# Performance work log

Hardware: AMD Instinct MI355X
Metric: run time of the kernel (lower is better)

Reference implementation:

```python
import jax, jax.numpy as jnp
import numpy as np

B, N_IN, K_OUT, C_IN, C_OUT = 32, 2048, 128, 16, 16
NUM_ITERS = 3


def squash_v1(x, axis):
    s2 = (x ** 2).sum(axis, keepdims=True)
    return (jnp.sqrt(s2) / (0.5 + s2)) * x


def setup_inputs() -> dict:
    key = jax.random.key(0)
    k1, k2, k3 = jax.random.split(key, 3)
    x = jax.random.normal(k1, (B, N_IN, C_IN), dtype=jnp.float32)
    y = jax.random.normal(k2, (B, K_OUT), dtype=jnp.float32)  # unused by forward
    labels = jnp.arange(K_OUT, dtype=jnp.int64)
    # xavier-uniform-ish init for W1 [N_in, K_out, out_ch, in_ch] (leading 1 dropped)
    bound = float(np.sqrt(6.0 / (C_IN + C_OUT)))
    W1 = jax.random.uniform(k3, (N_IN, K_OUT, C_OUT, C_IN), dtype=jnp.float32,
                            minval=-bound, maxval=bound)
    return {"x": x, "y": y, "labels": labels, "W1": W1}


def reference(x, y, labels, W1):
    # select output capsules, then u_hat[b,i,k,d] = sum_c W[i,k,d,c] * x[b,i,c]
    W = W1[:, labels]                                   # [N, K, D, C]
    u_hat = jnp.einsum('ikdc,bic->bikd', W, x)          # [B, N, K, D]
    u_sq = squash_v1(u_hat, axis=-1)                    # reused each iteration
    b = jnp.zeros(u_hat.shape[:3], dtype=u_hat.dtype)   # [B, N, K]
    v = None
    for i in range(NUM_ITERS):
        c = jax.nn.softmax(b, axis=2)                   # over output capsules
        c = c / c.sum(axis=1, keepdims=True)            # normalize over input caps
        v = squash_v1(jnp.einsum('bik,bikd->bkd', c, u_hat), axis=-1)  # [B, K, D]
        if i < NUM_ITERS - 1:
            dd = 1.0 - ((u_sq - v[:, None]) ** 2).sum(-1)  # [B, N, K]
            b = b + dd
    poses = v                                           # [B, K, D]
    activations = jnp.sqrt((poses ** 2).sum(-1))        # [B, K]
    return poses, activations
```

## Files before the change

### kernel.cpp

```cpp
#include <hip/hip_runtime.h>


typedef __attribute__((ext_vector_type(8))) short  s16x8;
typedef __attribute__((ext_vector_type(4))) float  f32x4;

__device__ __forceinline__ unsigned bf16rn(float f) {
    const unsigned u = __builtin_bit_cast(unsigned, f);
    return (u + 0x7fffu + ((u >> 16) & 1u)) >> 16;
}
__device__ __forceinline__ unsigned pack2rn(float a, float b) {
    return bf16rn(a) | (bf16rn(b) << 16);
}
__device__ __forceinline__ unsigned phi(float a, float b) {
    return (__builtin_bit_cast(unsigned, a) >> 16) | (__builtin_bit_cast(unsigned, b) & 0xffff0000u);
}
__device__ __forceinline__ unsigned plo(float a, float b) {
    const float la = a - __builtin_bit_cast(float, __builtin_bit_cast(unsigned, a) & 0xffff0000u);
    const float lb = b - __builtin_bit_cast(float, __builtin_bit_cast(unsigned, b) & 0xffff0000u);
    return pack2rn(la, lb);
}

__device__ __forceinline__ void pack_A(const float* __restrict__ xp, s16x8& A1, s16x8& A2) {
    const float4 x0 = *(const float4*)xp;
    const float4 x1 = *(const float4*)(xp + 4);
    uint4 h, l;
    h.x = phi(x0.x, x0.y); h.y = phi(x0.z, x0.w);
    h.z = phi(x1.x, x1.y); h.w = phi(x1.z, x1.w);
    l.x = plo(x0.x, x0.y); l.y = plo(x0.z, x0.w);
    l.z = plo(x1.x, x1.y); l.w = plo(x1.z, x1.w);
    A1 = __builtin_bit_cast(s16x8, h);
    A2 = __builtin_bit_cast(s16x8, l);
}

__device__ __forceinline__ s16x8 pack_B_f(const float4 w0, const float4 w1, bool sel) {
    const float f[8] = {w0.x, w0.y, w0.z, w0.w, w1.x, w1.y, w1.z, w1.w};
    float t[8];
#pragma unroll
    for (int j = 0; j < 8; ++j) {
        const float hf = __builtin_bit_cast(float, __builtin_bit_cast(unsigned, f[j]) & 0xffff0000u);
        t[j] = sel ? hf : (f[j] - hf);
    }
    uint4 bw;
    bw.x = pack2rn(t[0], t[1]);
    bw.y = pack2rn(t[2], t[3]);
    bw.z = pack2rn(t[4], t[5]);
    bw.w = pack2rn(t[6], t[7]);
    return __builtin_bit_cast(s16x8, bw);
}
__device__ __forceinline__ s16x8 pack_B(const float* __restrict__ wp, bool sel) {
    return pack_B_f(*(const float4*)wp, *(const float4*)(wp + 4), sel);
}

__global__ __launch_bounds__(256) void k_packX(const float* __restrict__ x,
                                               s16x8* __restrict__ xA)
{
    const int wid  = blockIdx.x * 4 + (threadIdx.x >> 6);
    const int lane = threadIdx.x & 63;
    const int i  = wid >> 1, bg = wid & 1;
    const int n  = lane & 15, q = lane >> 4;
    const int oct = (q & 1) * 8;
    s16x8 A1, A2;
    pack_A(x + ((size_t)(bg * 16 + n) * 2048 + i) * 16 + oct, A1, A2);
    s16x8* o = xA + ((size_t)wid * 64 + lane) * 2;
    o[0] = A1;
    o[1] = A2;
}

__global__ __launch_bounds__(256) void k_packWacc(const float* __restrict__ W,
                                                  const s16x8* __restrict__ xA,
                                                  s16x8* __restrict__ Wp,
                                                  float* __restrict__ out_sl)
{
    const int w    = blockIdx.x * 4 + (threadIdx.x >> 6);
    const int lane = threadIdx.x & 63;
    const int n    = lane & 15;
    const int q    = lane >> 4;
    const int oct  = (q & 1) * 8;
    const bool sel = (q < 2);
    const int k0    = (w & 63) * 2;
    const int slice = w >> 6;
    const int i0    = slice * 32;

    const f32x4 zero = {0.f, 0.f, 0.f, 0.f};
    f32x4 acc[2][2];
#pragma unroll
    for (int kp = 0; kp < 2; ++kp)
#pragma unroll
        for (int bg = 0; bg < 2; ++bg) acc[kp][bg] = zero;

    float4 rw0[2], rw1[2];
    s16x8 X1c[2], X2c[2];
    {
        const float* wp_ = W + (size_t)i0 * 32768 + (size_t)k0 * 256 + n * 16 + oct;
        rw0[0] = *(const float4*)wp_;          rw1[0] = *(const float4*)(wp_ + 4);
        rw0[1] = *(const float4*)(wp_ + 256);  rw1[1] = *(const float4*)(wp_ + 260);
        const s16x8* xp = xA + (size_t)i0 * 256 + (size_t)lane * 2;
        X1c[0] = xp[0];   X2c[0] = xp[1];
        X1c[1] = xp[128]; X2c[1] = xp[129];
    }

#pragma unroll 1
    for (int i = i0; i < i0 + 32; ++i) {
        const int in_ = (i + 1 < i0 + 32) ? i + 1 : i;
        float4 nw0[2], nw1[2];
        s16x8 X1n[2], X2n[2];
        {
            const float* wp_ = W + (size_t)in_ * 32768 + (size_t)k0 * 256 + n * 16 + oct;
            nw0[0] = *(const float4*)wp_;          nw1[0] = *(const float4*)(wp_ + 4);
            nw0[1] = *(const float4*)(wp_ + 256);  nw1[1] = *(const float4*)(wp_ + 260);
            const s16x8* xp = xA + (size_t)in_ * 256 + (size_t)lane * 2;
            X1n[0] = xp[0];   X2n[0] = xp[1];
            X1n[1] = xp[128]; X2n[1] = xp[129];
        }
#pragma unroll
        for (int kp = 0; kp < 2; ++kp) {
            const s16x8 Wf = pack_B_f(rw0[kp], rw1[kp], sel);
            Wp[((size_t)i * 128 + (k0 + kp)) * 64 + lane] = Wf;
#pragma unroll
            for (int bg = 0; bg < 2; ++bg) {
                acc[kp][bg] = __builtin_amdgcn_mfma_f32_16x16x32_bf16(Wf, X1c[bg], acc[kp][bg], 0, 0, 0);
                acc[kp][bg] = __builtin_amdgcn_mfma_f32_16x16x32_bf16(Wf, X2c[bg], acc[kp][bg], 0, 0, 0);
            }
        }
#pragma unroll
        for (int kp = 0; kp < 2; ++kp) { rw0[kp] = nw0[kp]; rw1[kp] = nw1[kp]; }
#pragma unroll
        for (int bg = 0; bg < 2; ++bg) { X1c[bg] = X1n[bg]; X2c[bg] = X2n[bg]; }
    }
#pragma unroll
    for (int kp = 0; kp < 2; ++kp)
#pragma unroll
        for (int bg = 0; bg < 2; ++bg)
            *(f32x4*)(out_sl + (((size_t)slice * 32 + bg * 16 + n) * 128 + (k0 + kp)) * 16 + 4 * q)
                = acc[kp][bg];
}

__global__ __launch_bounds__(1024) void k_iter(const s16x8* __restrict__ Wp,
                                               const s16x8* __restrict__ xA,
                                               const float* __restrict__ Vq,
                                               const float* __restrict__ Nt,
                                               const float T,
                                               float* __restrict__ out_sl,
                                               float* __restrict__ csl)
{
    __shared__ float den_s[16][16];
    __shared__ float denom_s[16];
    const int tid  = threadIdx.x;
    const int wv   = tid >> 6, lane = tid & 63;
    const int n    = lane & 15, q = lane >> 4;
    const int bid  = blockIdx.x;
    const int c    = (bid & 7) | ((bid >> 4) << 3);
    const int h    = (bid >> 3) & 1;
    const int i0    = c * 8;
    const int kbase = wv * 8;
    const f32x4 zero = {0.f, 0.f, 0.f, 0.f};

    f32x4 acc[8];
    float cs0[2] = {0.f, 0.f};
#pragma unroll
    for (int kp = 0; kp < 8; ++kp) acc[kp] = zero;

#pragma unroll 1
    for (int ii = 0; ii < 8; ++ii) {
        const int i = i0 + ii;
        const s16x8* xp = xA + (size_t)i * 256 + (size_t)lane * 2;
        const s16x8 X1 = xp[h * 128];
        const s16x8 X2 = xp[h * 128 + 1];
        const s16x8* wrow = Wp + ((size_t)i * 128 + kbase) * 64 + lane;

        s16x8 Wfs[8];
#pragma unroll
        for (int kp = 0; kp < 8; ++kp) Wfs[kp] = wrow[(size_t)kp * 64];

        float es[8];
        float den = 0.f;
#pragma unroll
        for (int kp = 0; kp < 8; ++kp) {
            const int k = kbase + kp;
            f32x4 u = __builtin_amdgcn_mfma_f32_16x16x32_bf16(Wfs[kp], X1, zero, 0, 0, 0);
            u       = __builtin_amdgcn_mfma_f32_16x16x32_bf16(Wfs[kp], X2, u,    0, 0, 0);
            const float4 Vv = *(const float4*)(Vq + (((size_t)k * 4 + q) * 32 + h * 16 + n) * 4);
            float s2 = u.x * u.x;
            s2 = fmaf(u.y, u.y, s2);
            s2 = fmaf(u.z, u.z, s2);
            s2 = fmaf(u.w, u.w, s2);
            float dt = u.x * Vv.x;
            dt = fmaf(u.y, Vv.y, dt);
            dt = fmaf(u.z, Vv.z, dt);
            dt = fmaf(u.w, Vv.w, dt);
            s2 += __shfl_xor(s2, 16, 64);
            s2 += __shfl_xor(s2, 32, 64);
            dt += __shfl_xor(dt, 16, 64);
            dt += __shfl_xor(dt, 32, 64);
            const float Nr  = Nt[(size_t)k * 32 + h * 16 + n];
            const float inv = 1.0f / (0.5f + s2);
            const float scl = sqrtf(s2) * inv;
            const float fq  = s2 * s2 * inv * inv;
            const float e   = __expf(T * (1.0f - fq) + 2.0f * scl * dt - Nr);
            es[kp] = e;
            den += e;
        }
        if (lane < 16) den_s[wv][n] = den;
        __syncthreads();
        if (tid < 16) {
            float s = 0.f;
#pragma unroll
            for (int w2 = 0; w2 < 16; ++w2) s += den_s[w2][tid];
            denom_s[tid] = s;
        }
        __syncthreads();
        const float inv0 = 1.0f / denom_s[n];
#pragma unroll
        for (int kp = 0; kp < 8; ++kp) {
            f32x4 u = __builtin_amdgcn_mfma_f32_16x16x32_bf16(Wfs[kp], X1, zero, 0, 0, 0);
            u       = __builtin_amdgcn_mfma_f32_16x16x32_bf16(Wfs[kp], X2, u,    0, 0, 0);
            const float p = es[kp] * inv0;
            acc[kp].x = fmaf(p, u.x, acc[kp].x);
            acc[kp].y = fmaf(p, u.y, acc[kp].y);
            acc[kp].z = fmaf(p, u.z, acc[kp].z);
            acc[kp].w = fmaf(p, u.w, acc[kp].w);
            if ((kp >> 1) == q) cs0[kp & 1] += p;
        }
        __syncthreads();
    }
#pragma unroll
    for (int kp = 0; kp < 8; ++kp)
        *(f32x4*)(out_sl + (((size_t)c * 32 + h * 16 + n) * 128 + (kbase + kp)) * 16 + 4 * q)
            = acc[kp];
#pragma unroll
    for (int j = 0; j < 2; ++j)
        csl[((size_t)c * 128 + kbase + 2 * q + j) * 32 + h * 16 + n] = cs0[j];
}

template<bool USE_P>
__global__ __launch_bounds__(256) void k_acc_fb(const float* __restrict__ W,
                                                const float* __restrict__ x,
                                                const float* __restrict__ p,
                                                float* __restrict__ out_sl,
                                                float* __restrict__ csl)
{
    const int w    = blockIdx.x * 4 + (threadIdx.x >> 6);
    const int lane = threadIdx.x & 63;
    const int n    = lane & 15;
    const int q    = lane >> 4;
    const int oct  = (q & 1) * 8;
    const bool sel = (q < 2);
    const int k0    = (w & 63) * 2;
    const int slice = w >> 6;
    const int i0    = slice * 32;

    const f32x4 zero = {0.f, 0.f, 0.f, 0.f};
    f32x4 acc[2][2];
    float csacc[2][2];
#pragma unroll
    for (int kp = 0; kp < 2; ++kp)
#pragma unroll
        for (int bg = 0; bg < 2; ++bg) { acc[kp][bg] = zero; csacc[kp][bg] = 0.f; }

#pragma unroll 1
    for (int i = i0; i < i0 + 32; ++i) {
        s16x8 X1[2], X2[2];
#pragma unroll
        for (int bg = 0; bg < 2; ++bg)
            pack_A(x + ((size_t)(bg * 16 + n) * 2048 + i) * 16 + oct, X1[bg], X2[bg]);
#pragma unroll
        for (int kp = 0; kp < 2; ++kp) {
            const int k = k0 + kp;
            const s16x8 Wf = pack_B(W + (size_t)i * 32768 + (size_t)k * 256 + n * 16 + oct, sel);
#pragma unroll
            for (int bg = 0; bg < 2; ++bg) {
                if (USE_P) {
                    f32x4 u = __builtin_amdgcn_mfma_f32_16x16x32_bf16(Wf, X1[bg], zero, 0, 0, 0);
                    u       = __builtin_amdgcn_mfma_f32_16x16x32_bf16(Wf, X2[bg], u,    0, 0, 0);
                    const float pv = p[((size_t)i * 128 + k) * 32 + bg * 16 + n];
                    acc[kp][bg].x = fmaf(pv, u.x, acc[kp][bg].x);
                    acc[kp][bg].y = fmaf(pv, u.y, acc[kp][bg].y);
                    acc[kp][bg].z = fmaf(pv, u.z, acc[kp][bg].z);
                    acc[kp][bg].w = fmaf(pv, u.w, acc[kp][bg].w);
                    csacc[kp][bg] += pv;
                } else {
                    acc[kp][bg] = __builtin_amdgcn_mfma_f32_16x16x32_bf16(Wf, X1[bg], acc[kp][bg], 0, 0, 0);
                    acc[kp][bg] = __builtin_amdgcn_mfma_f32_16x16x32_bf16(Wf, X2[bg], acc[kp][bg], 0, 0, 0);
                }
            }
        }
    }
#pragma unroll
    for (int kp = 0; kp < 2; ++kp)
#pragma unroll
        for (int bg = 0; bg < 2; ++bg)
            *(f32x4*)(out_sl + (((size_t)slice * 32 + bg * 16 + n) * 128 + (k0 + kp)) * 16 + 4 * q)
                = acc[kp][bg];
    if (USE_P && lane < 16) {
#pragma unroll
        for (int kp = 0; kp < 2; ++kp)
#pragma unroll
            for (int bg = 0; bg < 2; ++bg)
                csl[((size_t)slice * 128 + (k0 + kp)) * 32 + bg * 16 + n] = csacc[kp][bg];
    }
}

__global__ __launch_bounds__(512) void k_logits_fb(const float* __restrict__ W,
                                                   const float* __restrict__ x,
                                                   const float* __restrict__ Vq,
                                                   const float* __restrict__ Nt,
                                                   const float T,
                                                   float* __restrict__ pbuf)
{
    __shared__ __align__(16) float e_s[8][16][32];
    __shared__ __align__(16) float den_s[8][32];
    __shared__ float denom_s[32];
    const int tid  = threadIdx.x;
    const int wv   = tid >> 6, lane = tid & 63;
    const int n    = lane & 15, q = lane >> 4;
    const int oct  = (q & 1) * 8;
    const bool sel = (q < 2);
    const f32x4 zero = {0.f, 0.f, 0.f, 0.f};
    const int pk = tid >> 2;
    const int pb = (tid & 3) * 8;

    const int i0 = blockIdx.x * 4;
#pragma unroll 1
    for (int ii = 0; ii < 4; ++ii) {
        const int i = i0 + ii;
        s16x8 X1[2], X2[2];
#pragma unroll
        for (int bg = 0; bg < 2; ++bg)
            pack_A(x + ((size_t)(bg * 16 + n) * 2048 + i) * 16 + oct, X1[bg], X2[bg]);

        float den0 = 0.f, den1 = 0.f;
#pragma unroll
        for (int kp = 0; kp < 16; ++kp) {
            const int k = wv * 16 + kp;
            const s16x8 Wf = pack_B(W + (size_t)i * 32768 + (size_t)k * 256 + n * 16 + oct, sel);
            float ebg[2];
#pragma unroll
            for (int bg = 0; bg < 2; ++bg) {
                f32x4 u = __builtin_amdgcn_mfma_f32_16x16x32_bf16(Wf, X1[bg], zero, 0, 0, 0);
                u       = __builtin_amdgcn_mfma_f32_16x16x32_bf16(Wf, X2[bg], u,    0, 0, 0);
                const float4 Vv = *(const float4*)(Vq + (((size_t)k * 4 + q) * 32 + bg * 16 + n) * 4);
                float s2 = u.x * u.x;
                s2 = fmaf(u.y, u.y, s2);
                s2 = fmaf(u.z, u.z, s2);
                s2 = fmaf(u.w, u.w, s2);
                float dt = u.x * Vv.x;
                dt = fmaf(u.y, Vv.y, dt);
                dt = fmaf(u.z, Vv.z, dt);
                dt = fmaf(u.w, Vv.w, dt);
                s2 += __shfl_xor(s2, 16, 64);
                s2 += __shfl_xor(s2, 32, 64);
                dt += __shfl_xor(dt, 16, 64);
                dt += __shfl_xor(dt, 32, 64);
                const float Nr  = Nt[(size_t)k * 32 + bg * 16 + n];
                const float inv = 1.0f / (0.5f + s2);
                const float scl = sqrtf(s2) * inv;
                const float fq  = s2 * s2 * inv * inv;
                const float e   = __expf(T * (1.0f - fq) + 2.0f * scl * dt - Nr);
                if (bg == 0) den0 += e; else den1 += e;
                ebg[bg] = e;
            }
            if (lane < 16) {
                e_s[wv][kp][n]      = ebg[0];
                e_s[wv][kp][16 + n] = ebg[1];
            }
        }
        if (lane < 16) {
            den_s[wv][n]      = den0;
            den_s[wv][16 + n] = den1;
        }
        __syncthreads();
        if (tid < 32) {
            float s = 0.f;
#pragma unroll
            for (int w2 = 0; w2 < 8; ++w2) s += den_s[w2][tid];
            denom_s[tid] = s;
        }
        __syncthreads();
        {
            const float4 e0 = *(const float4*)&e_s[pk >> 4][pk & 15][pb];
            const float4 e1 = *(const float4*)&e_s[pk >> 4][pk & 15][pb + 4];
            const float4 d0 = *(const float4*)&denom_s[pb];
            const float4 d1 = *(const float4*)&denom_s[pb + 4];
            float4 p0, p1;
            p0.x = e0.x / d0.x; p0.y = e0.y / d0.y; p0.z = e0.z / d0.z; p0.w = e0.w / d0.w;
            p1.x = e1.x / d1.x; p1.y = e1.y / d1.y; p1.z = e1.z / d1.z; p1.w = e1.w / d1.w;
            *(float4*)(pbuf + ((size_t)i * 128 + pk) * 32 + pb)     = p0;
            *(float4*)(pbuf + ((size_t)i * 128 + pk) * 32 + pb + 4) = p1;
        }
        __syncthreads();
    }
}

__global__ __launch_bounds__(256) void k_fin(const float* __restrict__ raw_sl,
                                             const float* __restrict__ csl,
                                             const float* __restrict__ Vq_prev,
                                             const float* __restrict__ Nt_prev,
                                             float* __restrict__ Vq_out,
                                             float* __restrict__ Nt_out,
                                             float* __restrict__ out,
                                             const int mode,
                                             const int nslice)
{
    const int tid = threadIdx.x;
    const int t   = blockIdx.x * 16 + (tid >> 4);
    const int d   = tid & 15;
    const int b   = t >> 7, k = t & 127;
    float s = 0.f, cs = 0.f;
    if (mode == 0) {
#pragma unroll 4
        for (int sl = 0; sl < nslice; ++sl) s += raw_sl[(size_t)sl * 65536 + (size_t)t * 16 + d];
    } else {
#pragma unroll 4
        for (int sl = 0; sl < nslice; ++sl) {
            s  += raw_sl[(size_t)sl * 65536 + (size_t)t * 16 + d];
            cs += csl[(size_t)sl * 4096 + k * 32 + b];
        }
    }
    const float invcs = (mode == 0) ? (1.0f / 2048.0f) : 1.0f / cs;
    const float v = s * invcs;
    float s2 = v * v;
#pragma unroll
    for (int m = 1; m < 16; m <<= 1) s2 += __shfl_xor(s2, m, 64);
    const float inv = 1.0f / (0.5f + s2);
    const float scl = sqrtf(s2) * inv;
    const size_t vidx = (((size_t)k * 4 + (d >> 2)) * 32 + b) * 4 + (d & 3);
    if (mode == 0) {
        Vq_out[vidx] = scl * v;
        if (d == 0) Nt_out[(size_t)k * 32 + b] = s2 * scl * scl;
    } else if (mode == 1) {
        Vq_out[vidx] = Vq_prev[vidx] + scl * v;
        if (d == 0) Nt_out[(size_t)k * 32 + b] = Nt_prev[(size_t)k * 32 + b] + s2 * scl * scl;
    } else {
        out[(size_t)t * 16 + d] = scl * v;
        if (d == 0) out[65536 + t] = s2 * inv;
    }
}

extern "C" void kernel_launch(void* const* d_in, const int* in_sizes, int n_in,
                              void* d_out, int out_size, void* d_ws, size_t ws_size,
                              hipStream_t stream)
{
    const float* x = (const float*)d_in[0];
    const float* W = (const float*)d_in[3];

    float* ws    = (float*)d_ws;
    float* Vbt0  = ws;
    float* VSbt  = ws + 65536;
    float* N1t   = ws + 131072;
    float* N2t   = ws + 135168;
    float* csl   = ws + 139264;
    float* slces = ws + 1187840;

    s16x8* Wp = (s16x8*)(ws + 17965056);
    s16x8* xA = (s16x8*)((short*)Wp + (size_t)134217728);
    const size_t needed = (size_t)17965056 * 4
                        + (size_t)134217728 * 2
                        + (size_t)8388608 * 2;
    const bool pk = (ws_size >= needed);

    if (pk) {
        k_packX<<<1024, 256, 0, stream>>>(x, xA);
        k_packWacc<<<1024, 256, 0, stream>>>(W, xA, Wp, slces);
        k_fin<<<256, 256, 0, stream>>>(slces, nullptr, nullptr, nullptr, Vbt0, N1t, nullptr, 0, 64);
        k_iter<<<512, 1024, 0, stream>>>(Wp, xA, Vbt0, N1t, 1.0f, slces, csl);
        k_fin<<<256, 256, 0, stream>>>(slces, csl, Vbt0, N1t, VSbt, N2t, nullptr, 1, 256);
        k_iter<<<512, 1024, 0, stream>>>(Wp, xA, VSbt, N2t, 2.0f, slces, csl);
        k_fin<<<256, 256, 0, stream>>>(slces, csl, nullptr, nullptr, nullptr, nullptr, (float*)d_out, 2, 256);
    } else {
        float* pbuf = (float*)Wp;
        k_acc_fb<false><<<1024, 256, 0, stream>>>(W, x, nullptr, slces, nullptr);
        k_fin<<<256, 256, 0, stream>>>(slces, nullptr, nullptr, nullptr, Vbt0, N1t, nullptr, 0, 64);
        k_logits_fb<<<512, 512, 0, stream>>>(W, x, Vbt0, N1t, 1.0f, pbuf);
        k_acc_fb<true><<<1024, 256, 0, stream>>>(W, x, pbuf, slces, csl);
        k_fin<<<256, 256, 0, stream>>>(slces, csl, Vbt0, N1t, VSbt, N2t, nullptr, 1, 64);
        k_logits_fb<<<512, 512, 0, stream>>>(W, x, VSbt, N2t, 2.0f, pbuf);
        k_acc_fb<true><<<1024, 256, 0, stream>>>(W, x, pbuf, slces, csl);
        k_fin<<<256, 256, 0, stream>>>(slces, csl, nullptr, nullptr, nullptr, nullptr, (float*)d_out, 2, 64);
    }
}
```

Measured before the change: 825.6 us.

## Drop materialized packed-W buffer; repack W inside routing iterations, trim barriers

The first accumulation pass no longer writes a packed bf16 hi/lo copy of W to workspace. The routing-iteration kernel instead reads the original fp32 W and packs the MFMA operands on the fly. This removes a large global write and shrinks the workspace, at the cost of repeating the pack arithmetic in both iterations. The per-step denominator reduction now uses a double-buffered shared array that every thread sums directly, which removes two of the three block barriers per step. The slice-reduction loop unroll in the finalize kernel is also raised.

Result: slower. 1.269 ms (+53.7%).

```diff
diff --git a/kernel.cpp b/kernel.cpp
--- a/kernel.cpp
+++ b/kernel.cpp
@@ -66,10 +66,9 @@
     o[1] = A2;
 }
 
-__global__ __launch_bounds__(256) void k_packWacc(const float* __restrict__ W,
-                                                  const s16x8* __restrict__ xA,
-                                                  s16x8* __restrict__ Wp,
-                                                  float* __restrict__ out_sl)
+__global__ __launch_bounds__(256) void k_acc0(const float* __restrict__ W,
+                                              const s16x8* __restrict__ xA,
+                                              float* __restrict__ out_sl)
 {
     const int w    = blockIdx.x * 4 + (threadIdx.x >> 6);
     const int lane = threadIdx.x & 63;
@@ -115,7 +114,6 @@
 #pragma unroll
         for (int kp = 0; kp < 2; ++kp) {
             const s16x8 Wf = pack_B_f(rw0[kp], rw1[kp], sel);
-            Wp[((size_t)i * 128 + (k0 + kp)) * 64 + lane] = Wf;
 #pragma unroll
             for (int bg = 0; bg < 2; ++bg) {
                 acc[kp][bg] = __builtin_amdgcn_mfma_f32_16x16x32_bf16(Wf, X1c[bg], acc[kp][bg], 0, 0, 0);
@@ -135,7 +133,7 @@
                 = acc[kp][bg];
 }
 
-__global__ __launch_bounds__(1024) void k_iter(const s16x8* __restrict__ Wp,
+__global__ __launch_bounds__(1024) void k_iter(const float* __restrict__ W,
                                                const s16x8* __restrict__ xA,
                                                const float* __restrict__ Vq,
                                                const float* __restrict__ Nt,
@@ -143,11 +141,12 @@
                                                float* __restrict__ out_sl,
                                                float* __restrict__ csl)
 {
-    __shared__ float den_s[16][16];
-    __shared__ float denom_s[16];
+    __shared__ float den_s[2][16][16];
     const int tid  = threadIdx.x;
     const int wv   = tid >> 6, lane = tid & 63;
     const int n    = lane & 15, q = lane >> 4;
+    const int oct  = (q & 1) * 8;
+    const bool sel = (q < 2);
     const int bid  = blockIdx.x;
     const int c    = (bid & 7) | ((bid >> 4) << 3);
     const int h    = (bid >> 3) & 1;
@@ -166,11 +165,11 @@
         const s16x8* xp = xA + (size_t)i * 256 + (size_t)lane * 2;
         const s16x8 X1 = xp[h * 128];
         const s16x8 X2 = xp[h * 128 + 1];
-        const s16x8* wrow = Wp + ((size_t)i * 128 + kbase) * 64 + lane;
+        const float* wbase = W + (size_t)i * 32768 + (size_t)kbase * 256 + n * 16 + oct;
 
         s16x8 Wfs[8];
 #pragma unroll
-        for (int kp = 0; kp < 8; ++kp) Wfs[kp] = wrow[(size_t)kp * 64];
+        for (int kp = 0; kp < 8; ++kp) Wfs[kp] = pack_B(wbase + kp * 256, sel);
 
         float es[8];
         float den = 0.f;
@@ -200,16 +199,12 @@
             es[kp] = e;
             den += e;
         }
-        if (lane < 16) den_s[wv][n] = den;
+        if (lane < 16) den_s[ii & 1][wv][n] = den;
         __syncthreads();
-        if (tid < 16) {
-            float s = 0.f;
-#pragma unroll
-            for (int w2 = 0; w2 < 16; ++w2) s += den_s[w2][tid];
-            denom_s[tid] = s;
-        }
-        __syncthreads();
-        const float inv0 = 1.0f / denom_s[n];
+        float denom = 0.f;
+#pragma unroll
+        for (int w2 = 0; w2 < 16; ++w2) denom += den_s[ii & 1][w2][n];
+        const float inv0 = 1.0f / denom;
 #pragma unroll
         for (int kp = 0; kp < 8; ++kp) {
             f32x4 u = __builtin_amdgcn_mfma_f32_16x16x32_bf16(Wfs[kp], X1, zero, 0, 0, 0);
@@ -221,7 +216,6 @@
             acc[kp].w = fmaf(p, u.w, acc[kp].w);
             if ((kp >> 1) == q) cs0[kp & 1] += p;
         }
-        __syncthreads();
     }
 #pragma unroll
     for (int kp = 0; kp < 8; ++kp)
@@ -407,10 +401,10 @@
     const int b   = t >> 7, k = t & 127;
     float s = 0.f, cs = 0.f;
     if (mode == 0) {
-#pragma unroll 4
+#pragma unroll 8
         for (int sl = 0; sl < nslice; ++sl) s += raw_sl[(size_t)sl * 65536 + (size_t)t * 16 + d];
     } else {
-#pragma unroll 4
+#pragma unroll 8
         for (int sl = 0; sl < nslice; ++sl) {
             s  += raw_sl[(size_t)sl * 65536 + (size_t)t * 16 + d];
             cs += csl[(size_t)sl * 4096 + k * 32 + b];
@@ -451,23 +445,20 @@
     float* csl   = ws + 139264;
     float* slces = ws + 1187840;
 
-    s16x8* Wp = (s16x8*)(ws + 17965056);
-    s16x8* xA = (s16x8*)((short*)Wp + (size_t)134217728);
-    const size_t needed = (size_t)17965056 * 4
-                        + (size_t)134217728 * 2
-                        + (size_t)8388608 * 2;
+    s16x8* xA = (s16x8*)(ws + 17965056);
+    const size_t needed = (size_t)17965056 * 4 + (size_t)8388608;
     const bool pk = (ws_size >= needed);
 
     if (pk) {
         k_packX<<<1024, 256, 0, stream>>>(x, xA);
-        k_packWacc<<<1024, 256, 0, stream>>>(W, xA, Wp, slces);
+        k_acc0<<<1024, 256, 0, stream>>>(W, xA, slces);
         k_fin<<<256, 256, 0, stream>>>(slces, nullptr, nullptr, nullptr, Vbt0, N1t, nullptr, 0, 64);
-        k_iter<<<512, 1024, 0, stream>>>(Wp, xA, Vbt0, N1t, 1.0f, slces, csl);
+        k_iter<<<512, 1024, 0, stream>>>(W, xA, Vbt0, N1t, 1.0f, slces, csl);
         k_fin<<<256, 256, 0, stream>>>(slces, csl, Vbt0, N1t, VSbt, N2t, nullptr, 1, 256);
-        k_iter<<<512, 1024, 0, stream>>>(Wp, xA, VSbt, N2t, 2.0f, slces, csl);
+        k_iter<<<512, 1024, 0, stream>>>(W, xA, VSbt, N2t, 2.0f, slces, csl);
         k_fin<<<256, 256, 0, stream>>>(slces, csl, nullptr, nullptr, nullptr, nullptr, (float*)d_out, 2, 256);
     } else {
-        float* pbuf = (float*)Wp;
+        float* pbuf = ws + 5382144;
         k_acc_fb<false><<<1024, 256, 0, stream>>>(W, x, nullptr, slces, nullptr);
         k_fin<<<256, 256, 0, stream>>>(slces, nullptr, nullptr, nullptr, Vbt0, N1t, nullptr, 0, 64);
         k_logits_fb<<<512, 512, 0, stream>>>(W, x, Vbt0, N1t, 1.0f, pbuf);
```
